# Performance work log

Hardware: AMD Instinct MI355X
Metric: run time of the kernel (lower is better)

## Reference

```python
import jax, jax.numpy as jnp
import numpy as np

N_NODES = 100000
N_EDGES = 1600000
NUM_GRAPHS = 256
EMB = 10
Z = 32
K = 64


def setup_inputs() -> dict:
    key = jax.random.key(0)
    ks = jax.random.split(key, 8)
    x = jax.random.randint(ks[0], (N_NODES,), 0, N_NODES)
    edge_index = jax.random.randint(ks[1], (2, N_EDGES), 0, N_NODES)
    edge_weight = jax.random.uniform(ks[2], (N_EDGES,), dtype=jnp.float32)
    batch = jnp.sort(jax.random.randint(ks[3], (N_NODES,), 0, NUM_GRAPHS))
    embed_table = jax.random.normal(ks[4], (N_NODES, EMB), dtype=jnp.float32)
    W_conv = jax.random.normal(ks[5], (EMB, Z), dtype=jnp.float32) / np.sqrt(EMB)
    b_conv = jax.random.normal(ks[6], (Z,), dtype=jnp.float32) * 0.01
    W_read = jax.random.normal(ks[7], (Z, K), dtype=jnp.float32) / np.sqrt(Z)
    return {"x": x, "edge_index": edge_index, "edge_weight": edge_weight,
            "batch": batch, "embed_table": embed_table, "W_conv": W_conv,
            "b_conv": b_conv, "W_read": W_read}


def reference(x, edge_index, edge_weight, batch, embed_table, W_conv, b_conv, W_read):
    n = x.shape[0]
    # Embedding lookup (squeeze is a no-op for 1-D index input)
    h = embed_table[x]                       # [N, 10]
    # GCNConv with improved=True: linear transform first (small EMB->Z)
    h = h @ W_conv                           # [N, Z]
    # gcn_norm: add self-loops with fill value 2.0 (improved)
    row, col = edge_index[0], edge_index[1]
    loop = jnp.arange(n)
    row_f = jnp.concatenate([row, loop])
    col_f = jnp.concatenate([col, loop])
    w_f = jnp.concatenate([edge_weight, jnp.full((n,), 2.0, edge_weight.dtype)])
    deg = jax.ops.segment_sum(w_f, col_f, num_segments=n)        # [N]
    d_inv_sqrt = jnp.where(deg > 0, jax.lax.rsqrt(jnp.where(deg > 0, deg, 1.0)), 0.0)
    norm = d_inv_sqrt[row_f] * w_f * d_inv_sqrt[col_f]           # [E+N]
    # gather-scale-scatter: out[col] += norm * h[row]
    msgs = h[row_f] * norm[:, None]                              # [E+N, Z]
    out = jax.ops.segment_sum(msgs, col_f, num_segments=n) + b_conv  # [N, Z]
    # global_mean_pool over batch assignment
    sums = jax.ops.segment_sum(out, batch, num_segments=NUM_GRAPHS)      # [G, Z]
    cnts = jax.ops.segment_sum(jnp.ones((n,), out.dtype), batch, num_segments=NUM_GRAPHS)
    pooled = sums / jnp.maximum(cnts, 1.0)[:, None]              # [G, Z]
    logits = pooled @ W_read                                     # [G, K]
    return (pooled, logits)
```

## Files before the change

### kernel.cpp

```cpp
#include <hip/hip_runtime.h>
#include <hip/hip_fp16.h>

#define GG 256
#define ZZDIM 32
#define KK 64
#define EMBD 10
#define BPG 4
#define SGRID (GG * BPG)
#define SLOTS 64
#define SPG (BPG * SLOTS)
#define MAXN 4096
#define CAP 16384



__global__ void lb_kernel(const int* __restrict__ batch, int* __restrict__ lb,
                          int* __restrict__ gcur, int n) {
    int g = threadIdx.x;
    int lo = 0, hi = n;
    while (lo < hi) {
        int mid = (lo + hi) >> 1;
        if (batch[mid] < g) lo = mid + 1; else hi = mid;
    }
    lb[g] = lo;
    if (g == 0) lb[GG] = n;
    gcur[g] = g * CAP;
}

__global__ void __launch_bounds__(512) bucket_kernel(
    const int* __restrict__ row, const int* __restrict__ col, const float* __restrict__ w,
    const int* __restrict__ batch, const int* __restrict__ lb,
    int* __restrict__ gcur, float2* __restrict__ rec, int e) {
    __shared__ int lcnt[GG], lres[GG], loff[GG], lbs[GG];
    for (int t = threadIdx.x; t < GG; t += 512) { lcnt[t] = 0; loff[t] = 0; lbs[t] = lb[t]; }
    __syncthreads();
    const long start = (long)blockIdx.x * 8192;
    int myg[16]; unsigned myp[16];
#pragma unroll
    for (int k = 0; k < 16; ++k) {
        long i = start + k * 512 + threadIdx.x;
        int g = -1;
        if (i < e) {
            int c = col[i];
            g = batch[c];
            myp[k] = ((unsigned)(c - lbs[g]) << 17) | (unsigned)row[i];
            atomicAdd(&lcnt[g], 1);
        }
        myg[k] = g;
    }
    __syncthreads();
    for (int t = threadIdx.x; t < GG; t += 512)
        if (lcnt[t]) lres[t] = atomicAdd(&gcur[t], lcnt[t]);
    __syncthreads();
#pragma unroll
    for (int k = 0; k < 16; ++k) {
        long i = start + k * 512 + threadIdx.x;
        if (i < e) {
            int g = myg[k];
            int slot = lres[g] + atomicAdd(&loff[g], 1);
            rec[slot] = make_float2(w[i], __int_as_float((int)myp[k]));
        }
    }
}

__global__ void degB_kernel(const float2* __restrict__ rec, const int* __restrict__ gcur,
                            const int* __restrict__ lb, float* __restrict__ dinv) {
    __shared__ float dl[MAXN];
    const int g = blockIdx.x;
    const int ns = lb[g], ne = lb[g + 1], sz = ne - ns;
    const long lo = (long)g * CAP;
    const long hi = gcur[g];
    if (sz <= MAXN) {
        for (int t = threadIdx.x; t < sz; t += 256) dl[t] = 2.0f;
        __syncthreads();
        for (long it = lo + threadIdx.x; it < hi; it += 256) {
            float2 r = rec[it];
            atomicAdd(&dl[(unsigned)__float_as_int(r.y) >> 17], r.x);
        }
        __syncthreads();
        for (int t = threadIdx.x; t < sz; t += 256) dinv[ns + t] = rsqrtf(dl[t]);
    } else {
        for (int t = threadIdx.x; t < sz; t += 256) dinv[ns + t] = 2.0f;
        __syncthreads();
        for (long it = lo + threadIdx.x; it < hi; it += 256) {
            float2 r = rec[it];
            atomicAdd(&dinv[ns + ((unsigned)__float_as_int(r.y) >> 17)], r.x);
        }
        __syncthreads();
        for (int t = threadIdx.x; t < sz; t += 256) dinv[ns + t] = rsqrtf(dinv[ns + t]);
    }
}

__global__ void hs_kernel(const int* __restrict__ x, const float* __restrict__ emb,
                          const float* __restrict__ Wc, const float* __restrict__ dinv,
                          __half2* __restrict__ hs16, int n) {
    int tid = blockIdx.x * blockDim.x + threadIdx.x;
    int i = tid >> 4, zp = tid & 15;
    if (i >= n) return;
    float d = dinv[i];
    int xi = x[i];
    const float* er = emb + (long)xi * EMBD;
    float a0 = 0.f, a1 = 0.f;
#pragma unroll
    for (int j = 0; j < EMBD; ++j) {
        float ej = er[j];
        a0 += ej * Wc[j * ZZDIM + 2 * zp];
        a1 += ej * Wc[j * ZZDIM + 2 * zp + 1];
    }
    hs16[(long)i * 16 + zp] = __floats2half2_rn(d * a0, d * a1);
}

__global__ void __launch_bounds__(512) scatter_kernel(
    const float2* __restrict__ rec, const int* __restrict__ gcur,
    const int* __restrict__ lb, const float* __restrict__ dinv,
    const uint2* __restrict__ hsq, float* __restrict__ partial) {
    __shared__ float dl[MAXN];
    const int z4   = threadIdx.x & 7;
    const int slot = threadIdx.x >> 3;
    const int g = blockIdx.x >> 2;
    const int q = blockIdx.x & 3;
    const int sg = q * SLOTS + slot;
    const int ns = lb[g], ne = lb[g + 1], sz = ne - ns;
    const bool inl = (sz <= MAXN);
    if (inl) for (int t = threadIdx.x; t < sz; t += 512) dl[t] = dinv[ns + t];
    __syncthreads();

    float4 acc = make_float4(0.f, 0.f, 0.f, 0.f);

#define GATHER4(pp) hsq[(long)((pp) & 0x1FFFFu) * 8 + z4]
#define ACCUM(c, v) do {                                              \
        float2 f0 = __half22float2(*(const __half2*)&(v).x);          \
        float2 f1 = __half22float2(*(const __half2*)&(v).y);          \
        acc.x = fmaf((c), f0.x, acc.x); acc.y = fmaf((c), f0.y, acc.y);\
        acc.z = fmaf((c), f1.x, acc.z); acc.w = fmaf((c), f1.y, acc.w);\
    } while (0)

    const long lo = (long)g * CAP;
    const long hi = gcur[g];
    long it = lo + sg;
    for (; it + 3L * SPG < hi; it += 4L * SPG) {
        float2 r0 = rec[it];
        float2 r1 = rec[it + SPG];
        float2 r2 = rec[it + 2L * SPG];
        float2 r3 = rec[it + 3L * SPG];
        unsigned p0 = (unsigned)__float_as_int(r0.y), p1 = (unsigned)__float_as_int(r1.y);
        unsigned p2 = (unsigned)__float_as_int(r2.y), p3 = (unsigned)__float_as_int(r3.y);
        uint2 v0 = GATHER4(p0);
        uint2 v1 = GATHER4(p1);
        uint2 v2 = GATHER4(p2);
        uint2 v3 = GATHER4(p3);
        float c0 = r0.x * (inl ? dl[p0 >> 17] : dinv[ns + (p0 >> 17)]);
        float c1 = r1.x * (inl ? dl[p1 >> 17] : dinv[ns + (p1 >> 17)]);
        float c2 = r2.x * (inl ? dl[p2 >> 17] : dinv[ns + (p2 >> 17)]);
        float c3 = r3.x * (inl ? dl[p3 >> 17] : dinv[ns + (p3 >> 17)]);
        ACCUM(c0, v0); ACCUM(c1, v1); ACCUM(c2, v2); ACCUM(c3, v3);
    }
    for (; it < hi; it += SPG) {
        float2 r = rec[it];
        unsigned p = (unsigned)__float_as_int(r.y);
        uint2 v = GATHER4(p);
        float c = r.x * (inl ? dl[p >> 17] : dinv[ns + (p >> 17)]);
        ACCUM(c, v);
    }

    for (long i = ns + sg; i < ne; i += SPG) {
        float c2v = 2.0f * (inl ? dl[i - ns] : dinv[i]);
        uint2 v = hsq[i * 8 + z4];
        ACCUM(c2v, v);
    }
#undef GATHER4
#undef ACCUM

    __shared__ float4 s[SLOTS][8];
    __shared__ float4 s2[8][8];
    s[slot][z4] = acc;
    __syncthreads();
    if (threadIdx.x < 64) {
        int j = threadIdx.x & 7, part = threadIdx.x >> 3;
        float4 a = make_float4(0.f, 0.f, 0.f, 0.f);
#pragma unroll
        for (int k = 0; k < 8; ++k) {
            float4 b = s[part * 8 + k][j];
            a.x += b.x; a.y += b.y; a.z += b.z; a.w += b.w;
        }
        s2[part][j] = a;
    }
    __syncthreads();
    if (threadIdx.x < 8) {
        int j = threadIdx.x;
        float4 a = make_float4(0.f, 0.f, 0.f, 0.f);
#pragma unroll
        for (int k = 0; k < 8; ++k) {
            float4 b = s2[k][j];
            a.x += b.x; a.y += b.y; a.z += b.z; a.w += b.w;
        }
        *(float4*)&partial[(long)blockIdx.x * ZZDIM + j * 4] = a;
    }
}

__global__ void finalize_kernel(const float* __restrict__ partial, const int* __restrict__ lb,
                                const float* __restrict__ bc, const float* __restrict__ Wr,
                                float* __restrict__ out) {
    int g = blockIdx.x;
    int t = threadIdx.x;
    __shared__ float p[ZZDIM];
    if (t < ZZDIM) {
        float a = 0.f;
#pragma unroll
        for (int q = 0; q < BPG; ++q) a += partial[(long)(g * BPG + q) * ZZDIM + t];
        float c = (float)(lb[g + 1] - lb[g]);
        float v = (c > 0.f) ? (bc[t] + a / c) : 0.f;
        out[g * ZZDIM + t] = v;
        p[t] = v;
    }
    __syncthreads();
    float a = 0.f;
#pragma unroll
    for (int zz = 0; zz < ZZDIM; ++zz) a += p[zz] * Wr[zz * KK + t];
    out[GG * ZZDIM + g * KK + t] = a;
}


extern "C" void kernel_launch(void* const* d_in, const int* in_sizes, int n_in,
                              void* d_out, int out_size, void* d_ws, size_t ws_size,
                              hipStream_t stream) {
    const int*   x     = (const int*)d_in[0];
    const int*   ei    = (const int*)d_in[1];
    const float* ew    = (const float*)d_in[2];
    const int*   batch = (const int*)d_in[3];
    const float* emb   = (const float*)d_in[4];
    const float* Wc    = (const float*)d_in[5];
    const float* bc    = (const float*)d_in[6];
    const float* Wr    = (const float*)d_in[7];
    float* out = (float*)d_out;

    const int n = in_sizes[0];
    const int e = in_sizes[2];

    float* ws   = (float*)d_ws;
    __half2* hs16 = (__half2*)ws;
    float* dinv = ws + 16L * n;
    int*  lb    = (int*)(ws + 17L * n);
    int*  gcur  = lb + GG + 1;
    long rbase = 17L * n + (2 * GG + 1);
    rbase = (rbase + 63) & ~63L;
    float2* rec = (float2*)(ws + rbase);
    long pbase = rbase + 2L * GG * CAP;
    pbase = (pbase + 63) & ~63L;
    float* partial = ws + pbase;

    lb_kernel<<<1, 256, 0, stream>>>(batch, lb, gcur, n);
    bucket_kernel<<<(e + 8191) / 8192, 512, 0, stream>>>(ei, ei + e, ew, batch, lb, gcur, rec, e);
    degB_kernel<<<GG, 256, 0, stream>>>(rec, gcur, lb, dinv);
    hs_kernel<<<(n * 16 + 255) / 256, 256, 0, stream>>>(x, emb, Wc, dinv, hs16, n);
    scatter_kernel<<<SGRID, 512, 0, stream>>>(rec, gcur, lb, dinv, (const uint2*)hs16, partial);
    finalize_kernel<<<GG, KK, 0, stream>>>(partial, lb, bc, Wr, out);
}
```

Baseline: 85.04 us.

## Fuse degree+hs kernels, fold finalize into scatter, vectorize bucket loads

```diff
diff --git a/kernel.cpp b/kernel.cpp
--- a/kernel.cpp
+++ b/kernel.cpp
@@ -15,7 +15,7 @@
 
 
 __global__ void lb_kernel(const int* __restrict__ batch, int* __restrict__ lb,
-                          int* __restrict__ gcur, int n) {
+                          int* __restrict__ gcur, int* __restrict__ pcnt, int n) {
     int g = threadIdx.x;
     int lo = 0, hi = n;
     while (lo < hi) {
@@ -25,6 +25,7 @@
     lb[g] = lo;
     if (g == 0) lb[GG] = n;
     gcur[g] = g * CAP;
+    pcnt[g] = 0;
 }
 
 __global__ void __launch_bounds__(512) bucket_kernel(
@@ -32,44 +33,59 @@
     const int* __restrict__ batch, const int* __restrict__ lb,
     int* __restrict__ gcur, float2* __restrict__ rec, int e) {
     __shared__ int lcnt[GG], lres[GG], loff[GG], lbs[GG];
-    for (int t = threadIdx.x; t < GG; t += 512) { lcnt[t] = 0; loff[t] = 0; lbs[t] = lb[t]; }
-    __syncthreads();
-    const long start = (long)blockIdx.x * 8192;
-    int myg[16]; unsigned myp[16];
-#pragma unroll
-    for (int k = 0; k < 16; ++k) {
-        long i = start + k * 512 + threadIdx.x;
-        int g = -1;
-        if (i < e) {
-            int c = col[i];
-            g = batch[c];
-            myp[k] = ((unsigned)(c - lbs[g]) << 17) | (unsigned)row[i];
+    if (threadIdx.x < GG) { lcnt[threadIdx.x] = 0; loff[threadIdx.x] = 0; lbs[threadIdx.x] = lb[threadIdx.x]; }
+    __syncthreads();
+    const long i0 = (long)blockIdx.x * 2048 + threadIdx.x * 4;
+    int myg[4]; unsigned myp[4]; float myw[4];
+    if (i0 + 3 < e) {
+        int4  r4 = *(const int4*)(row + i0);
+        int4  c4 = *(const int4*)(col + i0);
+        float4 w4 = *(const float4*)(w + i0);
+        int cc[4] = {c4.x, c4.y, c4.z, c4.w};
+        int rr[4] = {r4.x, r4.y, r4.z, r4.w};
+        float wv[4] = {w4.x, w4.y, w4.z, w4.w};
+#pragma unroll
+        for (int k = 0; k < 4; ++k) {
+            int g = batch[cc[k]];
+            myg[k] = g; myw[k] = wv[k];
+            myp[k] = ((unsigned)(cc[k] - lbs[g]) << 17) | (unsigned)rr[k];
             atomicAdd(&lcnt[g], 1);
         }
-        myg[k] = g;
-    }
-    __syncthreads();
-    for (int t = threadIdx.x; t < GG; t += 512)
-        if (lcnt[t]) lres[t] = atomicAdd(&gcur[t], lcnt[t]);
-    __syncthreads();
-#pragma unroll
-    for (int k = 0; k < 16; ++k) {
-        long i = start + k * 512 + threadIdx.x;
-        if (i < e) {
-            int g = myg[k];
-            int slot = lres[g] + atomicAdd(&loff[g], 1);
-            rec[slot] = make_float2(w[i], __int_as_float((int)myp[k]));
-        }
-    }
-}
-
-__global__ void degB_kernel(const float2* __restrict__ rec, const int* __restrict__ gcur,
-                            const int* __restrict__ lb, float* __restrict__ dinv) {
+    } else {
+#pragma unroll
+        for (int k = 0; k < 4; ++k) {
+            long i = i0 + k;
+            myg[k] = -1;
+            if (i < e) {
+                int c = col[i];
+                int g = batch[c];
+                myg[k] = g; myw[k] = w[i];
+                myp[k] = ((unsigned)(c - lbs[g]) << 17) | (unsigned)row[i];
+                atomicAdd(&lcnt[g], 1);
+            }
+        }
+    }
+    __syncthreads();
+    if (threadIdx.x < GG && lcnt[threadIdx.x])
+        lres[threadIdx.x] = atomicAdd(&gcur[threadIdx.x], lcnt[threadIdx.x]);
+    __syncthreads();
+#pragma unroll
+    for (int k = 0; k < 4; ++k) {
+        if (myg[k] >= 0) {
+            int slot = lres[myg[k]] + atomicAdd(&loff[myg[k]], 1);
+            rec[slot] = make_float2(myw[k], __int_as_float((int)myp[k]));
+        }
+    }
+}
+
+__global__ void __launch_bounds__(256) deghs_kernel(
+    const float2* __restrict__ rec, const int* __restrict__ gcur, const int* __restrict__ lb,
+    const int* __restrict__ x, const float* __restrict__ emb, const float* __restrict__ Wc,
+    float* __restrict__ dinv, __half2* __restrict__ hs16) {
     __shared__ float dl[MAXN];
     const int g = blockIdx.x;
     const int ns = lb[g], ne = lb[g + 1], sz = ne - ns;
-    const long lo = (long)g * CAP;
-    const long hi = gcur[g];
+    const long lo = (long)g * CAP, hi = gcur[g];
     if (sz <= MAXN) {
         for (int t = threadIdx.x; t < sz; t += 256) dl[t] = 2.0f;
         __syncthreads();
@@ -78,7 +94,26 @@
             atomicAdd(&dl[(unsigned)__float_as_int(r.y) >> 17], r.x);
         }
         __syncthreads();
-        for (int t = threadIdx.x; t < sz; t += 256) dinv[ns + t] = rsqrtf(dl[t]);
+        for (int t = threadIdx.x; t < sz; t += 256) {
+            float d = rsqrtf(dl[t]);
+            dl[t] = d;
+            dinv[ns + t] = d;
+        }
+        __syncthreads();
+        for (int idx = threadIdx.x; idx < sz * 16; idx += 256) {
+            int iL = idx >> 4, zp = idx & 15;
+            int i = ns + iL;
+            float d = dl[iL];
+            const float* er = emb + (long)x[i] * EMBD;
+            float a0 = 0.f, a1 = 0.f;
+#pragma unroll
+            for (int j = 0; j < EMBD; ++j) {
+                float ej = er[j];
+                a0 += ej * Wc[j * ZZDIM + 2 * zp];
+                a1 += ej * Wc[j * ZZDIM + 2 * zp + 1];
+            }
+            hs16[(long)i * 16 + zp] = __floats2half2_rn(d * a0, d * a1);
+        }
     } else {
         for (int t = threadIdx.x; t < sz; t += 256) dinv[ns + t] = 2.0f;
         __syncthreads();
@@ -88,32 +123,29 @@
         }
         __syncthreads();
         for (int t = threadIdx.x; t < sz; t += 256) dinv[ns + t] = rsqrtf(dinv[ns + t]);
-    }
-}
-
-__global__ void hs_kernel(const int* __restrict__ x, const float* __restrict__ emb,
-                          const float* __restrict__ Wc, const float* __restrict__ dinv,
-                          __half2* __restrict__ hs16, int n) {
-    int tid = blockIdx.x * blockDim.x + threadIdx.x;
-    int i = tid >> 4, zp = tid & 15;
-    if (i >= n) return;
-    float d = dinv[i];
-    int xi = x[i];
-    const float* er = emb + (long)xi * EMBD;
-    float a0 = 0.f, a1 = 0.f;
-#pragma unroll
-    for (int j = 0; j < EMBD; ++j) {
-        float ej = er[j];
-        a0 += ej * Wc[j * ZZDIM + 2 * zp];
-        a1 += ej * Wc[j * ZZDIM + 2 * zp + 1];
-    }
-    hs16[(long)i * 16 + zp] = __floats2half2_rn(d * a0, d * a1);
+        __syncthreads();
+        for (int idx = threadIdx.x; idx < sz * 16; idx += 256) {
+            int iL = idx >> 4, zp = idx & 15;
+            int i = ns + iL;
+            float d = dinv[i];
+            const float* er = emb + (long)x[i] * EMBD;
+            float a0 = 0.f, a1 = 0.f;
+#pragma unroll
+            for (int j = 0; j < EMBD; ++j) {
+                float ej = er[j];
+                a0 += ej * Wc[j * ZZDIM + 2 * zp];
+                a1 += ej * Wc[j * ZZDIM + 2 * zp + 1];
+            }
+            hs16[(long)i * 16 + zp] = __floats2half2_rn(d * a0, d * a1);
+        }
+    }
 }
 
 __global__ void __launch_bounds__(512) scatter_kernel(
     const float2* __restrict__ rec, const int* __restrict__ gcur,
     const int* __restrict__ lb, const float* __restrict__ dinv,
-    const uint2* __restrict__ hsq, float* __restrict__ partial) {
+    const uint2* __restrict__ hsq, float* __restrict__ partial, int* __restrict__ pcnt,
+    const float* __restrict__ bc, const float* __restrict__ Wr, float* __restrict__ out) {
     __shared__ float dl[MAXN];
     const int z4   = threadIdx.x & 7;
     const int slot = threadIdx.x >> 3;
@@ -196,28 +228,35 @@
         }
         *(float4*)&partial[(long)blockIdx.x * ZZDIM + j * 4] = a;
     }
-}
-
-__global__ void finalize_kernel(const float* __restrict__ partial, const int* __restrict__ lb,
-                                const float* __restrict__ bc, const float* __restrict__ Wr,
-                                float* __restrict__ out) {
-    int g = blockIdx.x;
-    int t = threadIdx.x;
+
+    __shared__ int win;
     __shared__ float p[ZZDIM];
-    if (t < ZZDIM) {
+    __threadfence();
+    __syncthreads();
+    if (threadIdx.x == 0) {
+        win = (atomicAdd(&pcnt[g], 1) == BPG - 1) ? 1 : 0;
+        if (win) __threadfence();
+    }
+    __syncthreads();
+    if (!win) return;
+    if (threadIdx.x < ZZDIM) {
+        int t = threadIdx.x;
         float a = 0.f;
 #pragma unroll
-        for (int q = 0; q < BPG; ++q) a += partial[(long)(g * BPG + q) * ZZDIM + t];
-        float c = (float)(lb[g + 1] - lb[g]);
+        for (int qq = 0; qq < BPG; ++qq) a += partial[(long)(g * BPG + qq) * ZZDIM + t];
+        float c = (float)sz;
         float v = (c > 0.f) ? (bc[t] + a / c) : 0.f;
         out[g * ZZDIM + t] = v;
         p[t] = v;
     }
     __syncthreads();
-    float a = 0.f;
-#pragma unroll
-    for (int zz = 0; zz < ZZDIM; ++zz) a += p[zz] * Wr[zz * KK + t];
-    out[GG * ZZDIM + g * KK + t] = a;
+    if (threadIdx.x < KK) {
+        int t = threadIdx.x;
+        float a = 0.f;
+#pragma unroll
+        for (int zz = 0; zz < ZZDIM; ++zz) a += p[zz] * Wr[zz * KK + t];
+        out[GG * ZZDIM + g * KK + t] = a;
+    }
 }
 
 
@@ -242,17 +281,17 @@
     float* dinv = ws + 16L * n;
     int*  lb    = (int*)(ws + 17L * n);
     int*  gcur  = lb + GG + 1;
-    long rbase = 17L * n + (2 * GG + 1);
+    int*  pcnt  = gcur + GG;
+    long rbase = 17L * n + (3 * GG + 1);
     rbase = (rbase + 63) & ~63L;
     float2* rec = (float2*)(ws + rbase);
     long pbase = rbase + 2L * GG * CAP;
     pbase = (pbase + 63) & ~63L;
     float* partial = ws + pbase;
 
-    lb_kernel<<<1, 256, 0, stream>>>(batch, lb, gcur, n);
-    bucket_kernel<<<(e + 8191) / 8192, 512, 0, stream>>>(ei, ei + e, ew, batch, lb, gcur, rec, e);
-    degB_kernel<<<GG, 256, 0, stream>>>(rec, gcur, lb, dinv);
-    hs_kernel<<<(n * 16 + 255) / 256, 256, 0, stream>>>(x, emb, Wc, dinv, hs16, n);
-    scatter_kernel<<<SGRID, 512, 0, stream>>>(rec, gcur, lb, dinv, (const uint2*)hs16, partial);
-    finalize_kernel<<<GG, KK, 0, stream>>>(partial, lb, bc, Wr, out);
-}
+    lb_kernel<<<1, 256, 0, stream>>>(batch, lb, gcur, pcnt, n);
+    bucket_kernel<<<(e + 2047) / 2048, 512, 0, stream>>>(ei, ei + e, ew, batch, lb, gcur, rec, e);
+    deghs_kernel<<<GG, 256, 0, stream>>>(rec, gcur, lb, x, emb, Wc, dinv, hs16);
+    scatter_kernel<<<SGRID, 512, 0, stream>>>(rec, gcur, lb, dinv, (const uint2*)hs16,
+                                              partial, pcnt, bc, Wr, out);
+}
```

Measured after the change: 295.5 us. +247.5%, slower.
